# Kernel tuning notes

Measured on AMD Instinct MI355X. Metric: run time of the kernel, lower is better.

The kernel has to match this reference:

```python
import jax, jax.numpy as jnp
import numpy as np

NUM_CLASSES = 100
NUM_DIM = 384
BATCH = 4096


def setup_inputs() -> dict:
    key = jax.random.key(0)
    k1, k2, k3, k4 = jax.random.split(key, 4)
    inputs = jax.random.normal(k1, (BATCH, NUM_DIM), dtype=jnp.float32)
    targets = jax.random.randint(k2, (BATCH,), 0, NUM_CLASSES)
    centers = jax.random.normal(k3, (NUM_CLASSES, NUM_DIM), dtype=jnp.float32)
    centers_weights = jax.random.uniform(k4, (NUM_CLASSES, NUM_DIM), dtype=jnp.float32)
    return {
        "inputs": inputs,
        "targets": targets,
        "epoch_number": 0,
        "centers": centers,
        "centers_weights": centers_weights,
    }


def _closest_center_dist(centers, centers_weights):
    # calc_centers(which_one=1): dist[i,j] = sqrt(sum_d 2^w[i,d]*(c[i,d]-c[j,d])^2),
    # row-sorted, second-smallest (the diagonal 0 is the smallest).
    # Computed with numpy in the original -> detached constant.
    w = 2.0 ** centers_weights                      # [C, D]
    diff = centers[:, None, :] - centers[None, :, :]  # [C, C, D] (C=100, tiny)
    d2 = jnp.einsum('cd,ced->ce', w, diff * diff)   # [C, C]
    d = jnp.sqrt(d2)
    d = jnp.sort(d, axis=1)
    return jax.lax.stop_gradient(d[:, 1])           # [C]


def reference(inputs, targets, epoch_number, centers, centers_weights):
    B = inputs.shape[0]
    centers_dist = _closest_center_dist(centers, centers_weights)  # [C]

    c_b = centers[targets]                     # [B, D] centers_batch
    w_b = 2.0 ** centers_weights[targets]      # [B, D] weights (gathered)

    # dist[i, j] = sqrt( sum_d w_b[j,d] * (c_b[j,d] - inputs[i,d])^2 )
    # expanded into three contractions to avoid the [B,B,D] broadcast tensor
    t_cc = jnp.einsum('jd,jd->j', w_b, c_b * c_b)        # [B]   (j-term)
    t_xc = inputs @ (w_b * c_b).T                        # [B,B] cross term
    t_xx = (inputs * inputs) @ w_b.T                     # [B,B]
    d2 = t_cc[None, :] - 2.0 * t_xc + t_xx               # [B,B]
    dist = jnp.sqrt(jnp.maximum(d2, 1e-12))

    mask = targets[:, None] == targets[None, :]          # [B,B] same-class
    dist_ap = jnp.where(mask, dist, -jnp.inf).max(axis=1)  # hardest positive
    dist_an = jnp.where(mask, jnp.inf, dist).min(axis=1)   # hardest negative

    cc = centers_dist[targets]                           # [B]
    per_sample = dist_ap + jnp.where(dist_an >= cc, 0.0, cc - dist_an)
    return jnp.sum(per_sample) / B
```

## Files before the change

### kernel.cpp

```cpp
#include <hip/hip_runtime.h>
#include <math.h>

#define NC 100
#define ND 384
#define NB 4096
#define KS 4
#define KT 96
#define MT 32
#define XP 100
#define CPAD 33
#define PPAD 104
#define AUX 116
#define GEMM_BLOCKS (NB / MT * KS)

__global__ __launch_bounds__(256) void fused_kernel(
    const float* __restrict__ x, const float* __restrict__ centers,
    const float* __restrict__ cw, const int* __restrict__ targets,
    float* __restrict__ tcc, float* __restrict__ cdist,
    unsigned* __restrict__ pres16, float* __restrict__ part,
    float* __restrict__ out) {
  __shared__ float sA[MT * XP + 2 * NC * CPAD];
  int b = blockIdx.x, tid = threadIdx.x;
  int wave = tid >> 6, lane = tid & 63;

  if (b < NC) {
    int i = b;
    float* ci_s = sA;
    float* wi_s = sA + ND;
    float* sred = sA + 2 * ND;
    if (i == 0 && tid == 255) out[0] = 0.f;
    for (int d = tid; d < ND; d += 256) {
      ci_s[d] = centers[i * ND + d];
      wi_s[d] = exp2f(cw[i * ND + d]);
    }
    __syncthreads();
    {
      float p = 0.f;
      for (int d = tid; d < ND; d += 256) p = fmaf(wi_s[d] * ci_s[d], ci_s[d], p);
      #pragma unroll
      for (int off = 32; off; off >>= 1) p += __shfl_xor(p, off, 64);
      if (lane == 0) sred[wave] = p;
      __syncthreads();
      if (tid == 0) tcc[i] = sred[0] + sred[1] + sred[2] + sred[3];
      __syncthreads();
    }
    float minv = 1e30f;
    for (int s = 0; s < 24; s += 4) {
      float red[4];
      #pragma unroll
      for (int u = 0; u < 4; u++) {
        int j = wave + 4 * (s + u);
        float acc = 0.f;
        #pragma unroll
        for (int e = 0; e < 6; e++) {
          int d = lane + 64 * e;
          float df = ci_s[d] - centers[j * ND + d];
          acc = fmaf(wi_s[d] * df, df, acc);
        }
        red[u] = acc;
      }
      #pragma unroll
      for (int off = 32; off; off >>= 1) {
        #pragma unroll
        for (int u = 0; u < 4; u++) red[u] += __shfl_xor(red[u], off, 64);
      }
      #pragma unroll
      for (int u = 0; u < 4; u++) {
        int j = wave + 4 * (s + u);
        if (j != i) minv = fminf(minv, red[u]);
      }
    }
    {
      int j = wave + 96;
      float acc = 0.f;
      #pragma unroll
      for (int e = 0; e < 6; e++) {
        int d = lane + 64 * e;
        float df = ci_s[d] - centers[j * ND + d];
        acc = fmaf(wi_s[d] * df, df, acc);
      }
      #pragma unroll
      for (int off = 32; off; off >>= 1) acc += __shfl_xor(acc, off, 64);
      if (j != i) minv = fminf(minv, acc);
    }
    if (lane == 0) sred[wave] = minv;
    __syncthreads();
    if (tid == 0)
      cdist[i] = sqrtf(fminf(fminf(sred[0], sred[1]), fminf(sred[2], sred[3])));
  } else if (b < AUX) {
    int pb = b - NC;
    unsigned* um = (unsigned*)sA;
    if (tid < 4) um[tid] = 0u;
    __syncthreads();
    int t = targets[pb * 256 + tid];
    atomicOr(&um[t >> 5], 1u << (t & 31));
    __syncthreads();
    if (tid < 4) pres16[pb * 4 + tid] = um[tid];
  } else {
    int g = b - AUX;
    int mb = g >> 2, ks = g & 3;
    float* xs = sA;
    float* wcs = sA + MT * XP;
    float* acs = wcs + NC * CPAD;
    int koff0 = ks * KT;

    for (int j = tid; j < MT * KT / 4; j += 256) {
      int r = j / 24, c4 = j - r * 24;
      float4 v = *(const float4*)(x + (mb * MT + r) * ND + koff0 + c4 * 4);
      *(float4*)(&xs[r * XP + c4 * 4]) = v;
    }
    float cwr[13], ccr[13];
    #pragma unroll
    for (int j = 0; j < 13; j++) {
      int idx = tid + 256 * j;
      if (idx < NC * 32) {
        int k = idx >> 5, d = idx & 31;
        cwr[j] = cw[k * ND + koff0 + d];
        ccr[j] = centers[k * ND + koff0 + d];
      }
    }

    int cg = tid & 31, sg = tid >> 5;
    int ku[4];
    #pragma unroll
    for (int u = 0; u < 4; u++) ku[u] = min(cg + 32 * u, NC - 1);
    float acc[4][4];
    #pragma unroll
    for (int m = 0; m < 4; m++)
      #pragma unroll
      for (int u = 0; u < 4; u++) acc[m][u] = 0.f;

    for (int ch = 0; ch < 3; ch++) {
      __syncthreads();
      #pragma unroll
      for (int j = 0; j < 13; j++) {
        int idx = tid + 256 * j;
        if (idx < NC * 32) {
          int k = idx >> 5, d = idx & 31;
          float w = exp2f(cwr[j]);
          wcs[k * CPAD + d] = w;
          acs[k * CPAD + d] = w * ccr[j];
        }
      }
      __syncthreads();
      if (ch < 2) {
        int koff = koff0 + (ch + 1) * 32;
        #pragma unroll
        for (int j = 0; j < 13; j++) {
          int idx = tid + 256 * j;
          if (idx < NC * 32) {
            int k = idx >> 5, d = idx & 31;
            cwr[j] = cw[k * ND + koff + d];
            ccr[j] = centers[k * ND + koff + d];
          }
        }
      }
      int dbase = ch * 32;
      #pragma unroll 4
      for (int d = 0; d < 32; d++) {
        float wv[4], m2a[4];
        #pragma unroll
        for (int u = 0; u < 4; u++) {
          wv[u] = wcs[ku[u] * CPAD + d];
          m2a[u] = -2.f * acs[ku[u] * CPAD + d];
        }
        int dcol = dbase + d;
        #pragma unroll
        for (int m = 0; m < 4; m++) {
          float xv = xs[(sg + 8 * m) * XP + dcol];
          #pragma unroll
          for (int u = 0; u < 4; u++)
            acc[m][u] = fmaf(xv, fmaf(xv, wv[u], m2a[u]), acc[m][u]);
        }
      }
    }
    #pragma unroll
    for (int m = 0; m < 4; m++) {
      int i = mb * MT + sg + 8 * m;
      #pragma unroll
      for (int u = 0; u < 4; u++) {
        int k = cg + 32 * u;
        if (k < NC) part[(ks * NB + i) * PPAD + k] = acc[m][u];
      }
    }
  }
}

__global__ __launch_bounds__(256) void finish_kernel(
    const int* __restrict__ targets, const float* __restrict__ tcc,
    const float* __restrict__ cdist, const unsigned* __restrict__ pres16,
    const float* __restrict__ part, float* __restrict__ out) {
  __shared__ unsigned msk[4];
  __shared__ float r_an[2][2], r_ap[2][2], lsum[8];
  int tid = threadIdx.x;
  if (tid < 4) {
    unsigned m = 0;
    #pragma unroll
    for (int bb = 0; bb < 16; bb++) m |= pres16[bb * 4 + tid];
    msk[tid] = m;
  }
  int wave = tid >> 6, lane = tid & 63;
  int h = wave & 1, sl = wave >> 1;
  int k = h * 64 + lane;
  bool valid = k < NC;
  float base = valid ? tcc[k] : 0.f;
  __syncthreads();
  bool pres = valid && ((msk[k >> 5] >> (k & 31)) & 1u);

  for (int pass = 0; pass < 4; pass++) {
    int i = blockIdx.x * 8 + pass * 2 + sl;
    int ti = targets[i];
    float cand_an = 1e30f, cand_ap = 0.f;
    if (valid) {
      float d2 = base;
      #pragma unroll
      for (int s = 0; s < KS; s++) d2 += part[(s * NB + i) * PPAD + k];
      float dist = sqrtf(fmaxf(d2, 1e-12f));
      if (k == ti) cand_ap = dist;
      else if (pres) cand_an = dist;
    }
    #pragma unroll
    for (int off = 32; off; off >>= 1) {
      cand_an = fminf(cand_an, __shfl_xor(cand_an, off, 64));
      cand_ap = fmaxf(cand_ap, __shfl_xor(cand_ap, off, 64));
    }
    if (lane == 0) { r_an[sl][h] = cand_an; r_ap[sl][h] = cand_ap; }
    __syncthreads();
    if (tid < 2) {
      int isamp = blockIdx.x * 8 + pass * 2 + tid;
      float cc = cdist[targets[isamp]];
      float an = fminf(r_an[tid][0], r_an[tid][1]);
      float ap = fmaxf(r_ap[tid][0], r_ap[tid][1]);
      lsum[pass * 2 + tid] = ap + ((an >= cc) ? 0.f : cc - an);
    }
    __syncthreads();
  }
  if (tid == 0) {
    float t = 0.f;
    #pragma unroll
    for (int j = 0; j < 8; j++) t += lsum[j];
    atomicAdd(out, t * (1.0f / NB));
  }
}

extern "C" void kernel_launch(void* const* d_in, const int* in_sizes, int n_in,
                              void* d_out, int out_size, void* d_ws, size_t ws_size,
                              hipStream_t stream) {
  const float* inputs  = (const float*)d_in[0];
  const int*   targets = (const int*)d_in[1];
  const float* centers = (const float*)d_in[3];
  const float* cw      = (const float*)d_in[4];
  float* out = (float*)d_out;

  float* tcc       = (float*)d_ws;
  float* cdist     = tcc + 128;
  unsigned* pres16 = (unsigned*)(cdist + 128);
  float* part      = (float*)(pres16 + 64);

  fused_kernel<<<AUX + GEMM_BLOCKS, 256, 0, stream>>>(
      inputs, centers, cw, targets, tcc, cdist, pres16, part, out);
  finish_kernel<<<NB / 8, 256, 0, stream>>>(targets, tcc, cdist, pres16, part, out);
}
```

Before: 93.42 us.

## Retile GEMM stage with 12-way K split, transposed class-major LDS and float4 loads

Replaces the 4-way K split over 32-row tiles with a 12-way split over 64-row tiles, each block handling a single 32-wide K chunk. The center and weight tile is stored transposed (d-major, classes contiguous), so each thread reads 4 adjacent classes with float4 LDS loads and writes 4 partial results with one float4 store. The register double-buffer prefetch loop is removed, and the block now computes 8x4 accumulators instead of 4x4. This raises memory-level parallelism and ILP and cuts LDS instruction count. In exchange, the partial-sum buffer triples in size, so finish_kernel must read 12 partials per entry, and it was not updated in the visible change.

```diff
diff --git a/kernel.cpp b/kernel.cpp
--- a/kernel.cpp
+++ b/kernel.cpp
@@ -4,22 +4,23 @@
 #define NC 100
 #define ND 384
 #define NB 4096
-#define KS 4
-#define KT 96
-#define MT 32
-#define XP 100
-#define CPAD 33
+#define KS 12
+#define KTC 32
+#define MT 64
+#define NSLOT 128
+#define CLS_PAD 132
+#define XSP 36
 #define PPAD 104
 #define AUX 116
 #define GEMM_BLOCKS (NB / MT * KS)
 
-__global__ __launch_bounds__(256) void fused_kernel(
+__global__ __launch_bounds__(256, 3) void fused_kernel(
     const float* __restrict__ x, const float* __restrict__ centers,
     const float* __restrict__ cw, const int* __restrict__ targets,
     float* __restrict__ tcc, float* __restrict__ cdist,
     unsigned* __restrict__ pres16, float* __restrict__ part,
     float* __restrict__ out) {
-  __shared__ float sA[MT * XP + 2 * NC * CPAD];
+  __shared__ float sA[MT * XSP + 2 * KTC * CLS_PAD];
   int b = blockIdx.x, tid = threadIdx.x;
   int wave = tid >> 6, lane = tid & 63;
 
@@ -98,89 +99,69 @@
     if (tid < 4) pres16[pb * 4 + tid] = um[tid];
   } else {
     int g = b - AUX;
-    int mb = g >> 2, ks = g & 3;
-    float* xs = sA;
-    float* wcs = sA + MT * XP;
-    float* acs = wcs + NC * CPAD;
-    int koff0 = ks * KT;
-
-    for (int j = tid; j < MT * KT / 4; j += 256) {
-      int r = j / 24, c4 = j - r * 24;
-      float4 v = *(const float4*)(x + (mb * MT + r) * ND + koff0 + c4 * 4);
-      *(float4*)(&xs[r * XP + c4 * 4]) = v;
-    }
-    float cwr[13], ccr[13];
-    #pragma unroll
-    for (int j = 0; j < 13; j++) {
+    int mb = g / KS;
+    int ks = g - mb * KS;
+    int koff = ks * KTC;
+    float* xs   = sA;
+    float* ws_t = sA + MT * XSP;
+    float* as_t = ws_t + KTC * CLS_PAD;
+
+    #pragma unroll
+    for (int j = 0; j < 2; j++) {
       int idx = tid + 256 * j;
-      if (idx < NC * 32) {
-        int k = idx >> 5, d = idx & 31;
-        cwr[j] = cw[k * ND + koff0 + d];
-        ccr[j] = centers[k * ND + koff0 + d];
-      }
-    }
+      int r = idx >> 3, c4 = idx & 7;
+      float4 v = *(const float4*)(x + (mb * MT + r) * ND + koff + 4 * c4);
+      *(float4*)(&xs[r * XSP + 4 * c4]) = v;
+    }
+    #pragma unroll
+    for (int j = 0; j < 16; j++) {
+      int idx = tid + 256 * j;
+      int k = idx >> 5, d = idx & 31;
+      float w = 0.f, c = 0.f;
+      if (k < NC) {
+        w = exp2f(cw[k * ND + koff + d]);
+        c = centers[k * ND + koff + d];
+      }
+      ws_t[d * CLS_PAD + k] = w;
+      as_t[d * CLS_PAD + k] = -2.f * w * c;
+    }
+    __syncthreads();
 
     int cg = tid & 31, sg = tid >> 5;
-    int ku[4];
-    #pragma unroll
-    for (int u = 0; u < 4; u++) ku[u] = min(cg + 32 * u, NC - 1);
-    float acc[4][4];
-    #pragma unroll
-    for (int m = 0; m < 4; m++)
+    float acc[8][4];
+    #pragma unroll
+    for (int m = 0; m < 8; m++)
       #pragma unroll
       for (int u = 0; u < 4; u++) acc[m][u] = 0.f;
 
-    for (int ch = 0; ch < 3; ch++) {
-      __syncthreads();
-      #pragma unroll
-      for (int j = 0; j < 13; j++) {
-        int idx = tid + 256 * j;
-        if (idx < NC * 32) {
-          int k = idx >> 5, d = idx & 31;
-          float w = exp2f(cwr[j]);
-          wcs[k * CPAD + d] = w;
-          acs[k * CPAD + d] = w * ccr[j];
-        }
-      }
-      __syncthreads();
-      if (ch < 2) {
-        int koff = koff0 + (ch + 1) * 32;
+    for (int d4 = 0; d4 < KTC; d4 += 4) {
+      float wv[4][4], av[4][4], xv[8][4];
+      #pragma unroll
+      for (int i2 = 0; i2 < 4; i2++) {
+        *(float4*)&wv[i2][0] = *(const float4*)(&ws_t[(d4 + i2) * CLS_PAD + 4 * cg]);
+        *(float4*)&av[i2][0] = *(const float4*)(&as_t[(d4 + i2) * CLS_PAD + 4 * cg]);
+      }
+      #pragma unroll
+      for (int m = 0; m < 8; m++)
+        *(float4*)&xv[m][0] = *(const float4*)(&xs[(sg + 8 * m) * XSP + d4]);
+      #pragma unroll
+      for (int i2 = 0; i2 < 4; i2++) {
         #pragma unroll
-        for (int j = 0; j < 13; j++) {
-          int idx = tid + 256 * j;
-          if (idx < NC * 32) {
-            int k = idx >> 5, d = idx & 31;
-            cwr[j] = cw[k * ND + koff + d];
-            ccr[j] = centers[k * ND + koff + d];
+        for (int m = 0; m < 8; m++) {
+          float xval = xv[m][i2];
+          #pragma unroll
+          for (int u = 0; u < 4; u++) {
+            float t = fmaf(xval, wv[i2][u], av[i2][u]);
+            acc[m][u] = fmaf(xval, t, acc[m][u]);
           }
         }
       }
-      int dbase = ch * 32;
-      #pragma unroll 4
-      for (int d = 0; d < 32; d++) {
-        float wv[4], m2a[4];
-        #pragma unroll
-        for (int u = 0; u < 4; u++) {
-          wv[u] = wcs[ku[u] * CPAD + d];
-          m2a[u] = -2.f * acs[ku[u] * CPAD + d];
-        }
-        int dcol = dbase + d;
-        #pragma unroll
-        for (int m = 0; m < 4; m++) {
-          float xv = xs[(sg + 8 * m) * XP + dcol];
-          #pragma unroll
-          for (int u = 0; u < 4; u++)
-            acc[m][u] = fmaf(xv, fmaf(xv, wv[u], m2a[u]), acc[m][u]);
-        }
-      }
-    }
-    #pragma unroll
-    for (int m = 0; m < 4; m++) {
-      int i = mb * MT + sg + 8 * m;
-      #pragma unroll
-      for (int u = 0; u < 4; u++) {
-        int k = cg + 32 * u;
-        if (k < NC) part[(ks * NB + i) * PPAD + k] = acc[m][u];
+    }
+    if (cg < 25) {
+      #pragma unroll
+      for (int m = 0; m < 8; m++) {
+        int i = mb * MT + sg + 8 * m;
+        *(float4*)(&part[(ks * NB + i) * PPAD + 4 * cg]) = *(float4*)&acc[m][0];
       }
     }
   }
```

Measured after the change: 94.51 us. No clear change (+1.2%).
